# Kernel tuning notes

Hardware: AMD Instinct MI355X
Metric: run time of the kernel (lower is better)

## Reference

```python
import math
import jax, jax.numpy as jnp
import numpy as np

LLM = 4096
QB = 512
SAM = 256
H = W = 64
OUT = 256
HEADS = 4
DH = SAM // HEADS
EPS = 1e-5


def _ln(x, g, b):
    mu = jnp.mean(x, axis=-1, keepdims=True)
    var = jnp.mean(jnp.square(x - mu), axis=-1, keepdims=True)
    return (x - mu) * jax.lax.rsqrt(var + EPS) * g + b


def _conv3x3(x, w):
    # x: (N,C,H,W), w: (O,I,3,3), padding=1
    return jax.lax.conv_general_dilated(
        x, w, window_strides=(1, 1), padding='SAME',
        dimension_numbers=('NCHW', 'OIHW', 'NCHW'))


def setup_inputs() -> dict:
    key = jax.random.key(0)
    ks = jax.random.split(key, 20)
    n = lambda k, sh, s: (jax.random.normal(k, sh, dtype=jnp.float32) * s)
    inp = {
        'image_embed': n(ks[0], (8, SAM, H, W), 1.0),
        'ref_vec': n(ks[1], (8, 32, LLM), 1.0),
        'querybook_slots': n(ks[2], (8, 32, QB), 1.0),
        # parameters (torch Linear layout: (out, in); conv: (O,I,kh,kw))
        'q_proj_w': n(ks[3], (HEADS * DH, LLM), 1.0 / math.sqrt(LLM)),
        'k_proj_w': n(ks[4], (HEADS * DH, SAM, 1, 1), 1.0 / math.sqrt(SAM)),
        'fuser_w1': n(ks[5], (HEADS, HEADS, 3, 3), 1.0 / math.sqrt(HEADS * 9)),
        'fuser_b1': n(ks[6], (HEADS,), 0.01),
        'fuser_w2': n(ks[7], (1, HEADS, 3, 3), 1.0 / math.sqrt(HEADS * 9)),
        'fuser_b2': jnp.full((1,), -1.8, dtype=jnp.float32),
        'qb_proj_w': n(ks[8], (LLM, QB), 1.0 / math.sqrt(QB)),
        'rf_ln_g': jnp.ones((2 * LLM,), jnp.float32),
        'rf_ln_b': jnp.zeros((2 * LLM,), jnp.float32),
        'rf_lin_w': n(ks[9], (LLM, 2 * LLM), 1.0 / math.sqrt(2 * LLM)),
        'rf_lin_b': n(ks[10], (LLM,), 0.01),
        'cf_ln_g': jnp.ones((LLM,), jnp.float32),
        'cf_ln_b': jnp.zeros((LLM,), jnp.float32),
        'cf_w1': n(ks[11], (LLM // 2, LLM), 1.0 / math.sqrt(LLM)),
        'cf_b1': n(ks[12], (LLM // 2,), 0.01),
        'cf_w2': n(ks[13], (1, LLM // 2), 1.0 / math.sqrt(LLM // 2)),
        'cf_b2': n(ks[14], (1,), 0.01),
    }
    return inp


def reference(image_embed, ref_vec, querybook_slots, q_proj_w, k_proj_w,
              fuser_w1, fuser_b1, fuser_w2, fuser_b2, qb_proj_w,
              rf_ln_g, rf_ln_b, rf_lin_w, rf_lin_b,
              cf_ln_g, cf_ln_b, cf_w1, cf_b1, cf_w2, cf_b2):
    B, C, h, w = image_embed.shape
    K = ref_vec.shape[1]
    # querybook projection + ref fuse
    qb = jnp.einsum('bkq,lq->bkl', querybook_slots, qb_proj_w)  # (B,K,LLM)
    cat = jnp.concatenate([ref_vec, qb], axis=-1)               # (B,K,2*LLM)
    fused = jax.nn.silu(jnp.einsum('bkc,lc->bkl', _ln(cat, rf_ln_g, rf_ln_b), rf_lin_w) + rf_lin_b)
    # per-slot query heads
    Q = jnp.einsum('bkl,ol->bko', fused, q_proj_w).reshape(B, K, HEADS, DH)
    # 1x1 conv key map -> (B,HEADS,DH,H,W)
    Kmap = jnp.einsum('bcxy,oc->boxy', image_embed, k_proj_w.reshape(HEADS * DH, SAM))
    Kmap = Kmap.reshape(B, HEADS, DH, h, w)
    # fused contraction over d_head (original materialized (B,K,HEADS,DH,H,W))
    logits_64_heads = jnp.einsum('bkhd,bhdxy->bkhxy', Q, Kmap) / math.sqrt(DH)
    x = logits_64_heads.reshape(B * K, HEADS, h, w)
    x = jax.nn.silu(_conv3x3(x, fuser_w1) + fuser_b1[None, :, None, None])
    logits_64 = _conv3x3(x, fuser_w2) + fuser_b2[None, :, None, None]  # (B*K,1,64,64)
    # bilinear upsample, align_corners=False (half-pixel centers)
    up = jax.image.resize(logits_64, (B * K, 1, OUT, OUT), method='bilinear')
    ref_logits_256 = up.reshape(B, K, OUT, OUT)
    # confidence head
    cfh = jax.nn.silu(jnp.einsum('bkl,ol->bko', _ln(fused, cf_ln_g, cf_ln_b), cf_w1) + cf_b1)
    conf_logits = (jnp.einsum('bko,lo->bkl', cfh, cf_w2) + cf_b2).squeeze(-1)  # (B,K)
    return ref_logits_256, conf_logits
```

## Files before the change

kernel.cpp:

```cpp
#include <hip/hip_runtime.h>

#define EPS 1e-5f

typedef __bf16 bf16_t;
typedef __bf16 bf16x8 __attribute__((ext_vector_type(8)));
typedef __bf16 bf16x4 __attribute__((ext_vector_type(4)));
typedef float f32x4 __attribute__((ext_vector_type(4)));

__device__ __forceinline__ float silu_f(float x) { return x / (1.f + __expf(-x)); }

__device__ __forceinline__ float block_sum(float v, float* tmp) {
#pragma unroll
  for (int off = 32; off > 0; off >>= 1) v += __shfl_down(v, off);
  __syncthreads();
  if ((threadIdx.x & 63) == 0) tmp[threadIdx.x >> 6] = v;
  __syncthreads();
  return tmp[0] + tmp[1] + tmp[2] + tmp[3];
}

__global__ __launch_bounds__(256) void cast_k(
    const float* __restrict__ X, bf16_t* __restrict__ Y, int n8) {
  int i = blockIdx.x * 256 + threadIdx.x;
  if (i >= n8) return;
  float4 v0 = *(const float4*)(X + i * 8);
  float4 v1 = *(const float4*)(X + i * 8 + 4);
  bf16x8 o;
  o[0] = (bf16_t)v0.x; o[1] = (bf16_t)v0.y; o[2] = (bf16_t)v0.z; o[3] = (bf16_t)v0.w;
  o[4] = (bf16_t)v1.x; o[5] = (bf16_t)v1.y; o[6] = (bf16_t)v1.z; o[7] = (bf16_t)v1.w;
  *(bf16x8*)(Y + i * 8) = o;
}

__global__ __launch_bounds__(1024, 4) void gemm_wide(
    const bf16_t* __restrict__ A, const float* __restrict__ B,
    float* __restrict__ Cpart, int N, int K, int KS) {
  __shared__ bf16_t As[256][72];
  __shared__ bf16_t Bs[128][72];
  const int t = threadIdx.x;
  const int lane = t & 63;
  const int w = t >> 6;
  const int n0 = blockIdx.x * 128;
  const int kbeg = blockIdx.y * KS;
  const int nt = KS >> 6;
  const int ar = t >> 2, ac = (t & 3) * 16;
  const int br = t >> 3, bc = (t & 7) * 8;
  const bf16_t* Ap = A + (size_t)ar * K + kbeg + ac;
  const float* Bp = B + (size_t)(n0 + br) * K + kbeg + bc;

  bf16x8 a0A, a1A, a0B, a1B, a0C, a1C, a0D, a1D;
  float4 b0A, b1A, b0B, b1B, b0C, b1C, b0D, b1D;

#define LOADSET(S, k0)                            \
  a0##S = *(const bf16x8*)(Ap + (k0));            \
  a1##S = *(const bf16x8*)(Ap + (k0) + 8);        \
  b0##S = *(const float4*)(Bp + (k0));            \
  b1##S = *(const float4*)(Bp + (k0) + 4);

#define STORESET(S)                                                         \
  {                                                                         \
    *(bf16x8*)&As[ar][ac] = a0##S;                                          \
    *(bf16x8*)&As[ar][ac + 8] = a1##S;                                      \
    bf16x8 wv;                                                              \
    wv[0] = (bf16_t)b0##S.x; wv[1] = (bf16_t)b0##S.y;                       \
    wv[2] = (bf16_t)b0##S.z; wv[3] = (bf16_t)b0##S.w;                       \
    wv[4] = (bf16_t)b1##S.x; wv[5] = (bf16_t)b1##S.y;                       \
    wv[6] = (bf16_t)b1##S.z; wv[7] = (bf16_t)b1##S.w;                       \
    *(bf16x8*)&Bs[br][bc] = wv;                                             \
  }

#define BARRIER_PINNED                 \
  __builtin_amdgcn_sched_barrier(0);   \
  __builtin_amdgcn_s_barrier();        \
  __builtin_amdgcn_sched_barrier(0);

#define LGKM_BARRIER                                   \
  asm volatile("s_waitcnt lgkmcnt(0)" ::: "memory");   \
  BARRIER_PINNED

  f32x4 acc[4][2];
#pragma unroll
  for (int i = 0; i < 4; ++i)
#pragma unroll
    for (int j = 0; j < 2; ++j) acc[i][j] = f32x4{0.f, 0.f, 0.f, 0.f};

  const int wm = (w & 3) * 64;
  const int wn = (w >> 2) * 32;
  const int fr = lane & 15;
  const int kq = (lane >> 4) * 8;

  auto COMPUTE = [&]() {
#pragma unroll
    for (int kk = 0; kk < 64; kk += 32) {
      bf16x8 af[4], bg[2];
#pragma unroll
      for (int i = 0; i < 4; ++i)
        af[i] = *(const bf16x8*)&As[wm + 16 * i + fr][kk + kq];
#pragma unroll
      for (int j = 0; j < 2; ++j)
        bg[j] = *(const bf16x8*)&Bs[wn + 16 * j + fr][kk + kq];
#pragma unroll
      for (int i = 0; i < 4; ++i)
#pragma unroll
        for (int j = 0; j < 2; ++j)
          acc[i][j] = __builtin_amdgcn_mfma_f32_16x16x32_bf16(af[i], bg[j], acc[i][j], 0, 0, 0);
    }
  };

#define PHASE(s_, SET)                                         \
  COMPUTE();                                                   \
  BARRIER_PINNED                                               \
  if ((s_) + 1 < nt) { STORESET(SET) }                         \
  if ((s_) + 5 < nt) { LOADSET(SET, ((s_) + 5) * 64) }         \
  LGKM_BARRIER

  LOADSET(A, 0)
  LOADSET(B, 64)
  LOADSET(C, 128)
  LOADSET(D, 192)
  STORESET(A)
  if (4 < nt) { LOADSET(A, 256) }
  LGKM_BARRIER

  for (int s = 0; s < nt; s += 4) {
    PHASE(s, B)
    PHASE(s + 1, C)
    PHASE(s + 2, D)
    PHASE(s + 3, A)
  }
#undef LOADSET
#undef STORESET
#undef PHASE
#undef BARRIER_PINNED
#undef LGKM_BARRIER

  float* Cz = Cpart + (size_t)blockIdx.y * 256 * N;
  const int rh = (lane >> 4) * 4, col = lane & 15;
#pragma unroll
  for (int i = 0; i < 4; ++i)
#pragma unroll
    for (int j = 0; j < 2; ++j)
#pragma unroll
      for (int rr = 0; rr < 4; ++rr)
        Cz[(size_t)(wm + 16 * i + rh + rr) * N + n0 + wn + 16 * j + col] = acc[i][j][rr];
}

__global__ __launch_bounds__(256) void gemm_small(
    const bf16_t* __restrict__ A16, const float* __restrict__ B32, float* __restrict__ Cv,
    int M, int N, int K, int KS, int S) {
  __shared__ bf16_t As[64][72];
  __shared__ bf16_t Bs[64][72];
  const int t = threadIdx.x;
  const int lane = t & 63;
  const int w = t >> 6;
  const int s = blockIdx.z;
  const int n0 = blockIdx.x * 64;
  const int m0 = blockIdx.y * 64;
  const int kbeg = s * KS;

  f32x4 acc[2][2];
#pragma unroll
  for (int i = 0; i < 2; ++i)
#pragma unroll
    for (int j = 0; j < 2; ++j) acc[i][j] = f32x4{0.f, 0.f, 0.f, 0.f};

  const int wm = (w & 1) * 32, wn = (w >> 1) * 32;
  const int fr = lane & 15;
  const int kq = (lane >> 4) * 8;

  for (int k0 = kbeg; k0 < kbeg + KS; k0 += 64) {
    bf16x8 a8[2];
    float4 b4[4];
    {
      const int rr = t >> 2, c8 = (t & 3) * 8;
#pragma unroll
      for (int i = 0; i < 2; ++i)
        a8[i] = *(const bf16x8*)(A16 + (size_t)(m0 + rr) * K + k0 + c8 + 32 * i);
    }
    {
      const int rr = t >> 4, c4 = (t & 15) * 4;
#pragma unroll
      for (int i = 0; i < 4; ++i)
        b4[i] = *(const float4*)(B32 + (size_t)(n0 + rr + 16 * i) * K + k0 + c4);
    }
    __syncthreads();
    {
      const int rr = t >> 2, c8 = (t & 3) * 8;
#pragma unroll
      for (int i = 0; i < 2; ++i) *(bf16x8*)&As[rr][c8 + 32 * i] = a8[i];
    }
    {
      const int rr = t >> 4, c4 = (t & 15) * 4;
#pragma unroll
      for (int i = 0; i < 4; ++i) {
        bf16x4 v = {(bf16_t)b4[i].x, (bf16_t)b4[i].y, (bf16_t)b4[i].z, (bf16_t)b4[i].w};
        *(bf16x4*)&Bs[rr + 16 * i][c4] = v;
      }
    }
    __syncthreads();
#pragma unroll
    for (int kk = 0; kk < 64; kk += 32) {
      bf16x8 af[2], bg[2];
#pragma unroll
      for (int i = 0; i < 2; ++i) {
        af[i] = *(const bf16x8*)&As[wm + 16 * i + fr][kk + kq];
        bg[i] = *(const bf16x8*)&Bs[wn + 16 * i + fr][kk + kq];
      }
#pragma unroll
      for (int i = 0; i < 2; ++i)
#pragma unroll
        for (int j = 0; j < 2; ++j)
          acc[i][j] = __builtin_amdgcn_mfma_f32_16x16x32_bf16(af[i], bg[j], acc[i][j], 0, 0, 0);
    }
    __syncthreads();
  }

  const int rh = (lane >> 4) * 4;
  const int col = lane & 15;
#pragma unroll
  for (int i = 0; i < 2; ++i)
#pragma unroll
    for (int j = 0; j < 2; ++j)
#pragma unroll
      for (int rr = 0; rr < 4; ++rr)
        Cv[(size_t)s * M * N + (size_t)(m0 + wm + 16 * i + rh + rr) * N + n0 + wn + 16 * j + col] =
            acc[i][j][rr];
}

__global__ __launch_bounds__(256) void gemm_attn(
    const float* __restrict__ A, const float* __restrict__ B, bf16_t* __restrict__ C) {
  __shared__ bf16_t As[64][72];
  __shared__ bf16_t Bs[64][72];
  const int t = threadIdx.x;
  const int lane = t & 63;
  const int w = t >> 6;
  const int b = blockIdx.z;
  const int n0 = blockIdx.x * 64;
  const int m0 = blockIdx.y * 64;
  const float* Ab = A + (size_t)b * 32768;
  const float* Bb = B + (size_t)b * 1048576;

  f32x4 acc[2][2];
#pragma unroll
  for (int i = 0; i < 2; ++i)
#pragma unroll
    for (int j = 0; j < 2; ++j) acc[i][j] = f32x4{0.f, 0.f, 0.f, 0.f};

  const int wm = (w & 1) * 32, wn = (w >> 1) * 32;
  const int fr = lane & 15;
  const int kq = (lane >> 4) * 8;

  for (int k0 = 0; k0 < 256; k0 += 64) {
    {
      const int rr = t >> 4, c4 = (t & 15) * 4;
      float4 a4[4];
#pragma unroll
      for (int i = 0; i < 4; ++i)
        a4[i] = *(const float4*)(Ab + (size_t)(m0 + rr + 16 * i) * 256 + k0 + c4);
      __syncthreads();
#pragma unroll
      for (int i = 0; i < 4; ++i) {
        bf16x4 v = {(bf16_t)a4[i].x, (bf16_t)a4[i].y, (bf16_t)a4[i].z, (bf16_t)a4[i].w};
        *(bf16x4*)&As[rr + 16 * i][c4] = v;
      }
    }
    {
      const int kr = t >> 2, nc = (t & 3) * 16;
      float4 b4[4];
#pragma unroll
      for (int i = 0; i < 4; ++i)
        b4[i] = *(const float4*)(Bb + (size_t)(k0 + kr) * 4096 + n0 + nc + 4 * i);
#pragma unroll
      for (int i = 0; i < 4; ++i) {
        Bs[nc + 4 * i + 0][kr] = (bf16_t)b4[i].x;
        Bs[nc + 4 * i + 1][kr] = (bf16_t)b4[i].y;
        Bs[nc + 4 * i + 2][kr] = (bf16_t)b4[i].z;
        Bs[nc + 4 * i + 3][kr] = (bf16_t)b4[i].w;
      }
    }
    __syncthreads();
#pragma unroll
    for (int kk = 0; kk < 64; kk += 32) {
      bf16x8 af[2], bg[2];
#pragma unroll
      for (int i = 0; i < 2; ++i) {
        af[i] = *(const bf16x8*)&As[wm + 16 * i + fr][kk + kq];
        bg[i] = *(const bf16x8*)&Bs[wn + 16 * i + fr][kk + kq];
      }
#pragma unroll
      for (int i = 0; i < 2; ++i)
#pragma unroll
        for (int j = 0; j < 2; ++j)
          acc[i][j] = __builtin_amdgcn_mfma_f32_16x16x32_bf16(af[i], bg[j], acc[i][j], 0, 0, 0);
    }
    __syncthreads();
  }

  bf16_t* Cb = C + (size_t)b * 524288;
  const int rh = (lane >> 4) * 4, col = lane & 15;
#pragma unroll
  for (int i = 0; i < 2; ++i)
#pragma unroll
    for (int j = 0; j < 2; ++j)
#pragma unroll
      for (int rr = 0; rr < 4; ++rr)
        Cb[(size_t)(m0 + wm + 16 * i + rh + rr) * 4096 + n0 + wn + 16 * j + col] =
            (bf16_t)acc[i][j][rr];
}

template <int SILU_, int BIAS_>
__global__ __launch_bounds__(256) void reduce_k(
    const float* __restrict__ part, int S, long slice,
    const float* __restrict__ bias, float scale,
    float* __restrict__ outF, bf16_t* __restrict__ outB,
    int nmask, long total4) {
  long i4 = (long)blockIdx.x * 256 + threadIdx.x;
  if (i4 >= total4) return;
  long i = i4 * 4;
  float4 v = *(const float4*)(part + i);
  for (int s = 1; s < S; ++s) {
    float4 u = *(const float4*)(part + (size_t)s * slice + i);
    v.x += u.x; v.y += u.y; v.z += u.z; v.w += u.w;
  }
  v.x *= scale; v.y *= scale; v.z *= scale; v.w *= scale;
  if (BIAS_) {
    float4 bb = *(const float4*)(bias + (i & nmask));
    v.x += bb.x; v.y += bb.y; v.z += bb.z; v.w += bb.w;
  }
  if (SILU_) { v.x = silu_f(v.x); v.y = silu_f(v.y); v.z = silu_f(v.z); v.w = silu_f(v.w); }
  if (outF) *(float4*)(outF + i) = v;
  if (outB) {
    bf16x4 o = {(bf16_t)v.x, (bf16_t)v.y, (bf16_t)v.z, (bf16_t)v.w};
    *(bf16x4*)(outB + i) = o;
  }
}

__global__ __launch_bounds__(256) void ln_rows(
    const float* __restrict__ X1, const float* __restrict__ X2, int L1, int L2,
    const float* __restrict__ g, const float* __restrict__ bta, bf16_t* __restrict__ Y) {
  __shared__ float tmp[4];
  const int row = blockIdx.x;
  const int L = L1 + L2;
  const float* x1 = X1 + (size_t)row * L1;
  const float* x2 = X2 ? X2 + (size_t)row * L2 : nullptr;
  float s = 0.f, ss = 0.f;
  for (int i = threadIdx.x * 4; i < L1; i += 1024) {
    float4 v = *(const float4*)(x1 + i);
    s += v.x + v.y + v.z + v.w;
    ss += v.x * v.x + v.y * v.y + v.z * v.z + v.w * v.w;
  }
  for (int i = threadIdx.x * 4; i < L2; i += 1024) {
    float4 v = *(const float4*)(x2 + i);
    s += v.x + v.y + v.z + v.w;
    ss += v.x * v.x + v.y * v.y + v.z * v.z + v.w * v.w;
  }
  s = block_sum(s, tmp);
  ss = block_sum(ss, tmp);
  const float mu = s / (float)L;
  const float inv = rsqrtf(ss / (float)L - mu * mu + EPS);
  bf16_t* y = Y + (size_t)row * L;
  for (int i = threadIdx.x * 4; i < L1; i += 1024) {
    float4 v = *(const float4*)(x1 + i);
    float4 gv = *(const float4*)(g + i);
    float4 bv = *(const float4*)(bta + i);
    bf16x4 o = {(bf16_t)((v.x - mu) * inv * gv.x + bv.x),
                (bf16_t)((v.y - mu) * inv * gv.y + bv.y),
                (bf16_t)((v.z - mu) * inv * gv.z + bv.z),
                (bf16_t)((v.w - mu) * inv * gv.w + bv.w)};
    *(bf16x4*)(y + i) = o;
  }
  for (int i = threadIdx.x * 4; i < L2; i += 1024) {
    float4 v = *(const float4*)(x2 + i);
    float4 gv = *(const float4*)(g + L1 + i);
    float4 bv = *(const float4*)(bta + L1 + i);
    bf16x4 o = {(bf16_t)((v.x - mu) * inv * gv.x + bv.x),
                (bf16_t)((v.y - mu) * inv * gv.y + bv.y),
                (bf16_t)((v.z - mu) * inv * gv.z + bv.z),
                (bf16_t)((v.w - mu) * inv * gv.w + bv.w)};
    *(bf16x4*)(y + L1 + i) = o;
  }
}

__global__ __launch_bounds__(256) void qw_kernel(
    const float* __restrict__ Q, const float* __restrict__ kW, float* __restrict__ QW) {
  __shared__ float q[256];
  const int bk = blockIdx.x;
  q[threadIdx.x] = Q[(size_t)bk * 256 + threadIdx.x];
  __syncthreads();
  const int c = threadIdx.x;
#pragma unroll
  for (int h = 0; h < 4; ++h) {
    float s = 0.f;
#pragma unroll 8
    for (int d = 0; d < 64; ++d)
      s += q[(h << 6) + d] * kW[(size_t)(((h << 6) + d) << 8) + c];
    QW[((size_t)(bk * 4 + h) << 8) + c] = s;
  }
}

__global__ __launch_bounds__(256) void conv_fused(
    const bf16_t* __restrict__ X, const float* __restrict__ W1,
    const float* __restrict__ B1, const float* __restrict__ W2,
    const float* __restrict__ B2, float* __restrict__ O) {
  __shared__ bf16_t lg[16384];
  __shared__ bf16_t mid[16384];
  __shared__ float lg64[4096];
  __shared__ float wsh[180];
  const int t = threadIdx.x;
  const size_t base = (size_t)blockIdx.x * 16384;
#pragma unroll
  for (int i = 0; i < 8; ++i) {
    int o = (i * 256 + t) * 8;
    *(bf16x8*)&lg[o] = *(const bf16x8*)(X + base + o);
  }
  if (t < 144) wsh[t] = W1[t];
  else if (t < 180) wsh[t] = W2[t - 144];
  __syncthreads();
  const int px0 = (t & 15) * 4, py0 = (t >> 4) * 4;
  {
    float acc1[4][16];
#pragma unroll
    for (int oc = 0; oc < 4; ++oc) {
      float bb = B1[oc];
#pragma unroll
      for (int p = 0; p < 16; ++p) acc1[oc][p] = bb;
    }
#pragma unroll
    for (int c = 0; c < 4; ++c) {
      float p[6][6];
#pragma unroll
      for (int yy = 0; yy < 6; ++yy) {
        int gy = py0 + yy - 1;
#pragma unroll
        for (int xx = 0; xx < 6; ++xx) {
          int gx = px0 + xx - 1;
          p[yy][xx] = ((unsigned)gy < 64u && (unsigned)gx < 64u)
                          ? (float)lg[c * 4096 + gy * 64 + gx] : 0.f;
        }
      }
#pragma unroll
      for (int oc = 0; oc < 4; ++oc) {
        float wr[9];
#pragma unroll
        for (int k = 0; k < 9; ++k) wr[k] = wsh[oc * 36 + c * 9 + k];
#pragma unroll
        for (int y = 0; y < 4; ++y)
#pragma unroll
          for (int x = 0; x < 4; ++x)
            acc1[oc][y * 4 + x] +=
                wr[0] * p[y][x] + wr[1] * p[y][x + 1] + wr[2] * p[y][x + 2]
              + wr[3] * p[y + 1][x] + wr[4] * p[y + 1][x + 1] + wr[5] * p[y + 1][x + 2]
              + wr[6] * p[y + 2][x] + wr[7] * p[y + 2][x + 1] + wr[8] * p[y + 2][x + 2];
      }
    }
#pragma unroll
    for (int oc = 0; oc < 4; ++oc)
#pragma unroll
      for (int y = 0; y < 4; ++y) {
        bf16x4 o;
#pragma unroll
        for (int x = 0; x < 4; ++x) o[x] = (bf16_t)silu_f(acc1[oc][y * 4 + x]);
        *(bf16x4*)&mid[oc * 4096 + (py0 + y) * 64 + px0] = o;
      }
  }
  __syncthreads();
  {
    float acc2[16];
    float bb = B2[0];
#pragma unroll
    for (int p = 0; p < 16; ++p) acc2[p] = bb;
#pragma unroll
    for (int c = 0; c < 4; ++c) {
      float p[6][6];
#pragma unroll
      for (int yy = 0; yy < 6; ++yy) {
        int gy = py0 + yy - 1;
#pragma unroll
        for (int xx = 0; xx < 6; ++xx) {
          int gx = px0 + xx - 1;
          p[yy][xx] = ((unsigned)gy < 64u && (unsigned)gx < 64u)
                          ? (float)mid[c * 4096 + gy * 64 + gx] : 0.f;
        }
      }
      float wr[9];
#pragma unroll
      for (int k = 0; k < 9; ++k) wr[k] = wsh[144 + c * 9 + k];
#pragma unroll
      for (int y = 0; y < 4; ++y)
#pragma unroll
        for (int x = 0; x < 4; ++x)
          acc2[y * 4 + x] +=
              wr[0] * p[y][x] + wr[1] * p[y][x + 1] + wr[2] * p[y][x + 2]
            + wr[3] * p[y + 1][x] + wr[4] * p[y + 1][x + 1] + wr[5] * p[y + 1][x + 2]
            + wr[6] * p[y + 2][x] + wr[7] * p[y + 2][x + 1] + wr[8] * p[y + 2][x + 2];
    }
#pragma unroll
    for (int y = 0; y < 4; ++y)
#pragma unroll
      for (int x = 0; x < 4; ++x) lg64[(py0 + y) * 64 + px0 + x] = acc2[y * 4 + x];
  }
  __syncthreads();
  float* Ob = O + (size_t)blockIdx.x * 65536;
  for (int rr = 0; rr < 64; ++rr) {
    int p4 = rr * 256 + t;
    int oy = p4 >> 6, ox0 = (p4 & 63) * 4;
    float sy = oy * 0.25f - 0.375f;
    int y0 = (int)floorf(sy);
    float wy = sy - (float)y0;
    int y1 = min(y0 + 1, 63); y0 = max(y0, 0);
    const float* r0 = &lg64[y0 * 64];
    const float* r1 = &lg64[y1 * 64];
    float4 o;
#pragma unroll
    for (int q = 0; q < 4; ++q) {
      int ox = ox0 + q;
      float sx = ox * 0.25f - 0.375f;
      int x0 = (int)floorf(sx);
      float wx = sx - (float)x0;
      int x1 = min(x0 + 1, 63); x0 = max(x0, 0);
      float v0 = r0[x0] + wx * (r0[x1] - r0[x0]);
      float v1 = r1[x0] + wx * (r1[x1] - r1[x0]);
      ((float*)&o)[q] = v0 + wy * (v1 - v0);
    }
    *(float4*)(Ob + oy * 256 + ox0) = o;
  }
}

__global__ __launch_bounds__(256) void conf_k(
    const float* __restrict__ cfh, const float* __restrict__ w2,
    const float* __restrict__ b2, float* __restrict__ out) {
  __shared__ float tmp[4];
  const int row = blockIdx.x;
  float s = 0.f;
  for (int i = threadIdx.x; i < 2048; i += 256)
    s += cfh[(size_t)row * 2048 + i] * w2[i];
  s = block_sum(s, tmp);
  if (threadIdx.x == 0) out[row] = s + b2[0];
}

extern "C" void kernel_launch(void* const* d_in, const int* in_sizes, int n_in,
                              void* d_out, int out_size, void* d_ws, size_t ws_size,
                              hipStream_t stream) {
  const float* img    = (const float*)d_in[0];
  const float* refv   = (const float*)d_in[1];
  const float* qs     = (const float*)d_in[2];
  const float* qpw    = (const float*)d_in[3];
  const float* kpw    = (const float*)d_in[4];
  const float* fw1    = (const float*)d_in[5];
  const float* fb1    = (const float*)d_in[6];
  const float* fw2    = (const float*)d_in[7];
  const float* fb2    = (const float*)d_in[8];
  const float* qbw    = (const float*)d_in[9];
  const float* rlg    = (const float*)d_in[10];
  const float* rlb    = (const float*)d_in[11];
  const float* rlw    = (const float*)d_in[12];
  const float* rlbias = (const float*)d_in[13];
  const float* clg    = (const float*)d_in[14];
  const float* clb    = (const float*)d_in[15];
  const float* cw1    = (const float*)d_in[16];
  const float* cb1    = (const float*)d_in[17];
  const float* cw2    = (const float*)d_in[18];
  const float* cb2    = (const float*)d_in[19];
  float* out = (float*)d_out;
  char* W = (char*)d_ws;

  float*  partF = (float*)(W + 0);
  bf16_t* l64hb = (bf16_t*)(W + 0);
  float*  partC = (float*)(W + 0);
  bf16_t* catln = (bf16_t*)(W + 33554432);
  float*  fus   = (float*)(W + 33554432);
  float*  qbf   = (float*)(W + 37748736);
  bf16_t* fusb  = (bf16_t*)(W + 37748736);
  bf16_t* lnf   = (bf16_t*)(W + 37748736);
  float*  partQ = (float*)(W + 41943040);
  float*  part8 = (float*)(W + 41943040);
  float*  Qb    = (float*)(W + 44040192);
  float*  QW    = (float*)(W + 44302336);
  float*  cfh   = (float*)(W + 45350912);
  bf16_t* qsb   = (bf16_t*)(W + 47448064);

  dim3 b256(256);
  dim3 b1024(1024);

  cast_k<<<dim3(64), b256, 0, stream>>>(qs, qsb, 16384);
  gemm_wide<<<dim3(32, 2), b1024, 0, stream>>>(qsb, qbw, partQ, 4096, 512, 256);
  reduce_k<0, 0><<<dim3(1024), b256, 0, stream>>>(
      partQ, 2, 1048576L, nullptr, 1.f, qbf, nullptr, 0, 262144L);
  ln_rows<<<dim3(256), b256, 0, stream>>>(refv, qbf, 4096, 4096, rlg, rlb, catln);
  gemm_wide<<<dim3(32, 8), b1024, 0, stream>>>(catln, rlw, partF, 4096, 8192, 1024);
  reduce_k<1, 1><<<dim3(1024), b256, 0, stream>>>(
      partF, 8, 1048576L, rlbias, 1.f, fus, fusb, 4095, 262144L);
  gemm_small<<<dim3(4, 4, 8), b256, 0, stream>>>(fusb, qpw, part8, 256, 256, 4096, 512, 8);
  reduce_k<0, 0><<<dim3(64), b256, 0, stream>>>(
      part8, 8, 65536L, nullptr, 0.125f, Qb, nullptr, 0, 16384L);
  qw_kernel<<<dim3(256), b256, 0, stream>>>(Qb, kpw, QW);
  gemm_attn<<<dim3(64, 2, 8), b256, 0, stream>>>(QW, img, l64hb);
  conv_fused<<<dim3(256), b256, 0, stream>>>(l64hb, fw1, fb1, fw2, fb2, out);
  ln_rows<<<dim3(256), b256, 0, stream>>>(fus, nullptr, 4096, 0, clg, clb, lnf);
  gemm_wide<<<dim3(16, 16), b1024, 0, stream>>>(lnf, cw1, partC, 2048, 4096, 256);
  reduce_k<1, 1><<<dim3(512), b256, 0, stream>>>(
      partC, 16, 524288L, cb1, 1.f, cfh, nullptr, 2047, 131072L);
  conf_k<<<dim3(256), b256, 0, stream>>>(cfh, cw2, cb2, out + 16777216);
}
```

Measured before the change: 204.2 us.

## Store split-K partials in bf16, fuse fp32 cast into querybook GEMM, retile attn GEMM

```diff
diff --git a/kernel.cpp b/kernel.cpp
--- a/kernel.cpp
+++ b/kernel.cpp
@@ -18,21 +18,9 @@
   return tmp[0] + tmp[1] + tmp[2] + tmp[3];
 }
 
-__global__ __launch_bounds__(256) void cast_k(
-    const float* __restrict__ X, bf16_t* __restrict__ Y, int n8) {
-  int i = blockIdx.x * 256 + threadIdx.x;
-  if (i >= n8) return;
-  float4 v0 = *(const float4*)(X + i * 8);
-  float4 v1 = *(const float4*)(X + i * 8 + 4);
-  bf16x8 o;
-  o[0] = (bf16_t)v0.x; o[1] = (bf16_t)v0.y; o[2] = (bf16_t)v0.z; o[3] = (bf16_t)v0.w;
-  o[4] = (bf16_t)v1.x; o[5] = (bf16_t)v1.y; o[6] = (bf16_t)v1.z; o[7] = (bf16_t)v1.w;
-  *(bf16x8*)(Y + i * 8) = o;
-}
-
 __global__ __launch_bounds__(1024, 4) void gemm_wide(
     const bf16_t* __restrict__ A, const float* __restrict__ B,
-    float* __restrict__ Cpart, int N, int K, int KS) {
+    bf16_t* __restrict__ Cpart, int N, int K, int KS) {
   __shared__ bf16_t As[256][72];
   __shared__ bf16_t Bs[128][72];
   const int t = threadIdx.x;
@@ -129,10 +117,8 @@
 #undef LOADSET
 #undef STORESET
 #undef PHASE
-#undef BARRIER_PINNED
-#undef LGKM_BARRIER
-
-  float* Cz = Cpart + (size_t)blockIdx.y * 256 * N;
+
+  bf16_t* Cz = Cpart + (size_t)blockIdx.y * 256 * N;
   const int rh = (lane >> 4) * 4, col = lane & 15;
 #pragma unroll
   for (int i = 0; i < 4; ++i)
@@ -140,7 +126,85 @@
     for (int j = 0; j < 2; ++j)
 #pragma unroll
       for (int rr = 0; rr < 4; ++rr)
-        Cz[(size_t)(wm + 16 * i + rh + rr) * N + n0 + wn + 16 * j + col] = acc[i][j][rr];
+        Cz[(size_t)(wm + 16 * i + rh + rr) * N + n0 + wn + 16 * j + col] =
+            (bf16_t)acc[i][j][rr];
+}
+
+__global__ __launch_bounds__(1024) void gemm_wide_s(
+    const float* __restrict__ A, const float* __restrict__ B,
+    bf16_t* __restrict__ Cpart, int N, int K, int KS) {
+  __shared__ bf16_t As[256][72];
+  __shared__ bf16_t Bs[128][72];
+  const int t = threadIdx.x;
+  const int lane = t & 63;
+  const int w = t >> 6;
+  const int n0 = blockIdx.x * 128;
+  const int kbeg = blockIdx.y * KS;
+  const int nt = KS >> 6;
+  const int ar = t >> 2, ac = (t & 3) * 16;
+  const int br = t >> 3, bc = (t & 7) * 8;
+  const float* Ap = A + (size_t)ar * K + kbeg + ac;
+  const float* Bp = B + (size_t)(n0 + br) * K + kbeg + bc;
+
+  f32x4 acc[4][2];
+#pragma unroll
+  for (int i = 0; i < 4; ++i)
+#pragma unroll
+    for (int j = 0; j < 2; ++j) acc[i][j] = f32x4{0.f, 0.f, 0.f, 0.f};
+
+  const int wm = (w & 3) * 64;
+  const int wn = (w >> 2) * 32;
+  const int fr = lane & 15;
+  const int kq = (lane >> 4) * 8;
+
+  for (int s = 0; s < nt; ++s) {
+    float4 av[4], bv[2];
+#pragma unroll
+    for (int i = 0; i < 4; ++i) av[i] = *(const float4*)(Ap + s * 64 + 4 * i);
+#pragma unroll
+    for (int i = 0; i < 2; ++i) bv[i] = *(const float4*)(Bp + s * 64 + 4 * i);
+    __syncthreads();
+    {
+      bf16x8 wa0, wa1, wb;
+      wa0[0] = (bf16_t)av[0].x; wa0[1] = (bf16_t)av[0].y; wa0[2] = (bf16_t)av[0].z; wa0[3] = (bf16_t)av[0].w;
+      wa0[4] = (bf16_t)av[1].x; wa0[5] = (bf16_t)av[1].y; wa0[6] = (bf16_t)av[1].z; wa0[7] = (bf16_t)av[1].w;
+      wa1[0] = (bf16_t)av[2].x; wa1[1] = (bf16_t)av[2].y; wa1[2] = (bf16_t)av[2].z; wa1[3] = (bf16_t)av[2].w;
+      wa1[4] = (bf16_t)av[3].x; wa1[5] = (bf16_t)av[3].y; wa1[6] = (bf16_t)av[3].z; wa1[7] = (bf16_t)av[3].w;
+      wb[0] = (bf16_t)bv[0].x; wb[1] = (bf16_t)bv[0].y; wb[2] = (bf16_t)bv[0].z; wb[3] = (bf16_t)bv[0].w;
+      wb[4] = (bf16_t)bv[1].x; wb[5] = (bf16_t)bv[1].y; wb[6] = (bf16_t)bv[1].z; wb[7] = (bf16_t)bv[1].w;
+      *(bf16x8*)&As[ar][ac] = wa0;
+      *(bf16x8*)&As[ar][ac + 8] = wa1;
+      *(bf16x8*)&Bs[br][bc] = wb;
+    }
+    __syncthreads();
+#pragma unroll
+    for (int kk = 0; kk < 64; kk += 32) {
+      bf16x8 af[4], bg[2];
+#pragma unroll
+      for (int i = 0; i < 4; ++i)
+        af[i] = *(const bf16x8*)&As[wm + 16 * i + fr][kk + kq];
+#pragma unroll
+      for (int j = 0; j < 2; ++j)
+        bg[j] = *(const bf16x8*)&Bs[wn + 16 * j + fr][kk + kq];
+#pragma unroll
+      for (int i = 0; i < 4; ++i)
+#pragma unroll
+        for (int j = 0; j < 2; ++j)
+          acc[i][j] = __builtin_amdgcn_mfma_f32_16x16x32_bf16(af[i], bg[j], acc[i][j], 0, 0, 0);
+    }
+    __syncthreads();
+  }
+
+  bf16_t* Cz = Cpart + (size_t)blockIdx.y * 256 * N;
+  const int rh = (lane >> 4) * 4, col = lane & 15;
+#pragma unroll
+  for (int i = 0; i < 4; ++i)
+#pragma unroll
+    for (int j = 0; j < 2; ++j)
+#pragma unroll
+      for (int rr = 0; rr < 4; ++rr)
+        Cz[(size_t)(wm + 16 * i + rh + rr) * N + n0 + wn + 16 * j + col] =
+            (bf16_t)acc[i][j][rr];
 }
 
 __global__ __launch_bounds__(256) void gemm_small(
@@ -225,16 +289,15 @@
             acc[i][j][rr];
 }
 
-__global__ __launch_bounds__(256) void gemm_attn(
+__global__ __launch_bounds__(512) void gemm_attn(
     const float* __restrict__ A, const float* __restrict__ B, bf16_t* __restrict__ C) {
-  __shared__ bf16_t As[64][72];
+  __shared__ bf16_t As[128][72];
   __shared__ bf16_t Bs[64][72];
   const int t = threadIdx.x;
   const int lane = t & 63;
   const int w = t >> 6;
-  const int b = blockIdx.z;
+  const int b = blockIdx.y;
   const int n0 = blockIdx.x * 64;
-  const int m0 = blockIdx.y * 64;
   const float* Ab = A + (size_t)b * 32768;
   const float* Bb = B + (size_t)b * 1048576;
 
@@ -244,37 +307,34 @@
 #pragma unroll
     for (int j = 0; j < 2; ++j) acc[i][j] = f32x4{0.f, 0.f, 0.f, 0.f};
 
-  const int wm = (w & 1) * 32, wn = (w >> 1) * 32;
+  const int wm = (w & 3) * 32;
+  const int wn = (w >> 2) * 32;
   const int fr = lane & 15;
   const int kq = (lane >> 4) * 8;
 
   for (int k0 = 0; k0 < 256; k0 += 64) {
-    {
-      const int rr = t >> 4, c4 = (t & 15) * 4;
-      float4 a4[4];
-#pragma unroll
-      for (int i = 0; i < 4; ++i)
-        a4[i] = *(const float4*)(Ab + (size_t)(m0 + rr + 16 * i) * 256 + k0 + c4);
-      __syncthreads();
-#pragma unroll
-      for (int i = 0; i < 4; ++i) {
-        bf16x4 v = {(bf16_t)a4[i].x, (bf16_t)a4[i].y, (bf16_t)a4[i].z, (bf16_t)a4[i].w};
-        *(bf16x4*)&As[rr + 16 * i][c4] = v;
-      }
-    }
-    {
-      const int kr = t >> 2, nc = (t & 3) * 16;
-      float4 b4[4];
-#pragma unroll
-      for (int i = 0; i < 4; ++i)
-        b4[i] = *(const float4*)(Bb + (size_t)(k0 + kr) * 4096 + n0 + nc + 4 * i);
-#pragma unroll
-      for (int i = 0; i < 4; ++i) {
-        Bs[nc + 4 * i + 0][kr] = (bf16_t)b4[i].x;
-        Bs[nc + 4 * i + 1][kr] = (bf16_t)b4[i].y;
-        Bs[nc + 4 * i + 2][kr] = (bf16_t)b4[i].z;
-        Bs[nc + 4 * i + 3][kr] = (bf16_t)b4[i].w;
-      }
+    const int r = t >> 2, c4 = (t & 3) * 16;
+    float4 a4[4];
+#pragma unroll
+    for (int i = 0; i < 4; ++i)
+      a4[i] = *(const float4*)(Ab + (size_t)r * 256 + k0 + c4 + 4 * i);
+    const int kr = t >> 3, nc = (t & 7) * 8;
+    float4 b4[2];
+#pragma unroll
+    for (int i = 0; i < 2; ++i)
+      b4[i] = *(const float4*)(Bb + (size_t)(k0 + kr) * 4096 + n0 + nc + 4 * i);
+    __syncthreads();
+#pragma unroll
+    for (int i = 0; i < 4; ++i) {
+      bf16x4 v = {(bf16_t)a4[i].x, (bf16_t)a4[i].y, (bf16_t)a4[i].z, (bf16_t)a4[i].w};
+      *(bf16x4*)&As[r][c4 + 4 * i] = v;
+    }
+#pragma unroll
+    for (int i = 0; i < 2; ++i) {
+      Bs[nc + 4 * i + 0][kr] = (bf16_t)b4[i].x;
+      Bs[nc + 4 * i + 1][kr] = (bf16_t)b4[i].y;
+      Bs[nc + 4 * i + 2][kr] = (bf16_t)b4[i].z;
+      Bs[nc + 4 * i + 3][kr] = (bf16_t)b4[i].w;
     }
     __syncthreads();
 #pragma unroll
@@ -302,16 +362,52 @@
     for (int j = 0; j < 2; ++j)
 #pragma unroll
       for (int rr = 0; rr < 4; ++rr)
-        Cb[(size_t)(m0 + wm + 16 * i + rh + rr) * 4096 + n0 + wn + 16 * j + col] =
+        Cb[(size_t)(wm + 16 * i + rh + rr) * 4096 + n0 + wn + 16 * j + col] =
             (bf16_t)acc[i][j][rr];
 }
 
 template <int SILU_, int BIAS_>
-__global__ __launch_bounds__(256) void reduce_k(
-    const float* __restrict__ part, int S, long slice,
+__global__ __launch_bounds__(256) void reduce_b(
+    const bf16_t* __restrict__ part, int S, long slice,
     const float* __restrict__ bias, float scale,
     float* __restrict__ outF, bf16_t* __restrict__ outB,
-    int nmask, long total4) {
+    long nmask, long total8) {
+  long i8 = (long)blockIdx.x * 256 + threadIdx.x;
+  if (i8 >= total8) return;
+  long i = i8 * 8;
+  float a[8] = {0.f, 0.f, 0.f, 0.f, 0.f, 0.f, 0.f, 0.f};
+  for (int s = 0; s < S; ++s) {
+    bf16x8 v = *(const bf16x8*)(part + (size_t)s * slice + i);
+#pragma unroll
+    for (int j = 0; j < 8; ++j) a[j] += (float)v[j];
+  }
+#pragma unroll
+  for (int j = 0; j < 8; ++j) a[j] *= scale;
+  if (BIAS_) {
+    const float* bb = bias + (i & nmask);
+#pragma unroll
+    for (int j = 0; j < 8; ++j) a[j] += bb[j];
+  }
+  if (SILU_) {
+#pragma unroll
+    for (int j = 0; j < 8; ++j) a[j] = silu_f(a[j]);
+  }
+  if (outF) {
+    float4 o0 = {a[0], a[1], a[2], a[3]}, o1 = {a[4], a[5], a[6], a[7]};
+    *(float4*)(outF + i) = o0;
+    *(float4*)(outF + i + 4) = o1;
+  }
+  if (outB) {
+    bf16x8 o;
+#pragma unroll
+    for (int j = 0; j < 8; ++j) o[j] = (bf16_t)a[j];
+    *(bf16x8*)(outB + i) = o;
+  }
+}
+
+__global__ __launch_bounds__(256) void reduce_k(
+    const float* __restrict__ part, int S, long slice, float scale,
+    float* __restrict__ outF, long total4) {
   long i4 = (long)blockIdx.x * 256 + threadIdx.x;
   if (i4 >= total4) return;
   long i = i4 * 4;
@@ -321,16 +417,7 @@
     v.x += u.x; v.y += u.y; v.z += u.z; v.w += u.w;
   }
   v.x *= scale; v.y *= scale; v.z *= scale; v.w *= scale;
-  if (BIAS_) {
-    float4 bb = *(const float4*)(bias + (i & nmask));
-    v.x += bb.x; v.y += bb.y; v.z += bb.z; v.w += bb.w;
-  }
-  if (SILU_) { v.x = silu_f(v.x); v.y = silu_f(v.y); v.z = silu_f(v.z); v.w = silu_f(v.w); }
-  if (outF) *(float4*)(outF + i) = v;
-  if (outB) {
-    bf16x4 o = {(bf16_t)v.x, (bf16_t)v.y, (bf16_t)v.z, (bf16_t)v.w};
-    *(bf16x4*)(outB + i) = o;
-  }
+  *(float4*)(outF + i) = v;
 }
 
 __global__ __launch_bounds__(256) void ln_rows(
@@ -562,41 +649,37 @@
   float* out = (float*)d_out;
   char* W = (char*)d_ws;
 
-  float*  partF = (float*)(W + 0);
+  bf16_t* partF = (bf16_t*)(W + 0);
   bf16_t* l64hb = (bf16_t*)(W + 0);
-  float*  partC = (float*)(W + 0);
-  bf16_t* catln = (bf16_t*)(W + 33554432);
-  float*  fus   = (float*)(W + 33554432);
-  float*  qbf   = (float*)(W + 37748736);
-  bf16_t* fusb  = (bf16_t*)(W + 37748736);
-  bf16_t* lnf   = (bf16_t*)(W + 37748736);
-  float*  partQ = (float*)(W + 41943040);
-  float*  part8 = (float*)(W + 41943040);
+  bf16_t* partC = (bf16_t*)(W + 0);
+  bf16_t* catln = (bf16_t*)(W + 16777216);
+  float*  fus   = (float*)(W + 16777216);
+  float*  qbf   = (float*)(W + 20971520);
+  bf16_t* fusb  = (bf16_t*)(W + 20971520);
+  bf16_t* lnf   = (bf16_t*)(W + 20971520);
+  bf16_t* partQ = (bf16_t*)(W + 25165824);
+  float*  part8 = (float*)(W + 25165824);
   float*  Qb    = (float*)(W + 44040192);
   float*  QW    = (float*)(W + 44302336);
   float*  cfh   = (float*)(W + 45350912);
-  bf16_t* qsb   = (bf16_t*)(W + 47448064);
 
   dim3 b256(256);
-  dim3 b1024(1024);
-
-  cast_k<<<dim3(64), b256, 0, stream>>>(qs, qsb, 16384);
-  gemm_wide<<<dim3(32, 2), b1024, 0, stream>>>(qsb, qbw, partQ, 4096, 512, 256);
-  reduce_k<0, 0><<<dim3(1024), b256, 0, stream>>>(
-      partQ, 2, 1048576L, nullptr, 1.f, qbf, nullptr, 0, 262144L);
+
+  gemm_wide_s<<<dim3(32, 8), dim3(1024), 0, stream>>>(qs, qbw, partQ, 4096, 512, 64);
+  reduce_b<0, 0><<<dim3(512), b256, 0, stream>>>(
+      partQ, 8, 1048576L, nullptr, 1.f, qbf, nullptr, 0L, 131072L);
   ln_rows<<<dim3(256), b256, 0, stream>>>(refv, qbf, 4096, 4096, rlg, rlb, catln);
-  gemm_wide<<<dim3(32, 8), b1024, 0, stream>>>(catln, rlw, partF, 4096, 8192, 1024);
-  reduce_k<1, 1><<<dim3(1024), b256, 0, stream>>>(
-      partF, 8, 1048576L, rlbias, 1.f, fus, fusb, 4095, 262144L);
+  gemm_wide<<<dim3(32, 8), dim3(1024), 0, stream>>>(catln, rlw, partF, 4096, 8192, 1024);
+  reduce_b<1, 1><<<dim3(512), b256, 0, stream>>>(
+      partF, 8, 1048576L, rlbias, 1.f, fus, fusb, 4095L, 131072L);
   gemm_small<<<dim3(4, 4, 8), b256, 0, stream>>>(fusb, qpw, part8, 256, 256, 4096, 512, 8);
-  reduce_k<0, 0><<<dim3(64), b256, 0, stream>>>(
-      part8, 8, 65536L, nullptr, 0.125f, Qb, nullptr, 0, 16384L);
+  reduce_k<<<dim3(64), b256, 0, stream>>>(part8, 8, 65536L, 0.125f, Qb, 16384L);
   qw_kernel<<<dim3(256), b256, 0, stream>>>(Qb, kpw, QW);
-  gemm_attn<<<dim3(64, 2, 8), b256, 0, stream>>>(QW, img, l64hb);
+  gemm_attn<<<dim3(64, 8), dim3(512), 0, stream>>>(QW, img, l64hb);
   conv_fused<<<dim3(256), b256, 0, stream>>>(l64hb, fw1, fb1, fw2, fb2, out);
   ln_rows<<<dim3(256), b256, 0, stream>>>(fus, nullptr, 4096, 0, clg, clb, lnf);
-  gemm_wide<<<dim3(16, 16), b1024, 0, stream>>>(lnf, cw1, partC, 2048, 4096, 256);
-  reduce_k<1, 1><<<dim3(512), b256, 0, stream>>>(
-      partC, 16, 524288L, cb1, 1.f, cfh, nullptr, 2047, 131072L);
+  gemm_wide<<<dim3(16, 16), dim3(1024), 0, stream>>>(lnf, cw1, partC, 2048, 4096, 256);
+  reduce_b<1, 1><<<dim3(256), b256, 0, stream>>>(
+      partC, 16, 524288L, cb1, 1.f, cfh, nullptr, 2047L, 65536L);
   conf_k<<<dim3(256), b256, 0, stream>>>(cfh, cw2, cb2, out + 16777216);
 }
```

New measurement: 195.0 us. 1.05x faster.
